# Kernel optimization log

Measured on AMD Instinct MI355X. Metric: run time of the kernel, lower is better.

The kernel has to match this reference:

```python
import jax, jax.numpy as jnp
import numpy as np

NUM_EMBEDDINGS = 1024
EMBEDDING_DIM = 256
COMMITMENT_COST = 0.25


def setup_inputs() -> dict:
    key = jax.random.key(0)
    k1, k2 = jax.random.split(key)
    inputs = jax.random.normal(k1, (64, 1024, EMBEDDING_DIM), dtype=jnp.float32)
    # codebook initialized uniform(-1/K, 1/K) as in the torch module
    embedding = jax.random.uniform(
        k2, (NUM_EMBEDDINGS, EMBEDDING_DIM), dtype=jnp.float32,
        minval=-1.0 / NUM_EMBEDDINGS, maxval=1.0 / NUM_EMBEDDINGS)
    return {"inputs": inputs, "embedding": embedding}


def reference(inputs, embedding):
    # flatten to [N, D]
    D = embedding.shape[1]
    flat = inputs.reshape(-1, D)
    distances = (jnp.sum(flat * flat, axis=1, keepdims=True)
                 + jnp.sum(embedding * embedding, axis=1)
                 - 2.0 * jnp.matmul(flat, embedding.T))
    encoding_indices = jnp.argmin(distances, axis=1)  # [N]
    # one_hot @ embedding == gather; use gather (same math, no NxK one-hot)
    quantized = jnp.take(embedding, encoding_indices, axis=0).reshape(inputs.shape)
    # commitment loss: mse(stop_grad(quantized), inputs)
    e_latent_loss = jnp.mean(jnp.square(jax.lax.stop_gradient(quantized) - inputs))
    loss = COMMITMENT_COST * e_latent_loss
    # straight-through estimator
    quantized = inputs + jax.lax.stop_gradient(quantized - inputs)
    return quantized, loss, encoding_indices.reshape(inputs.shape[:-1])
```

## Files before the change

### kernel.cpp

```cpp
#include <hip/hip_runtime.h>
#include <cfloat>
#include <climits>

#define N_ROWS 65536
#define DIM 256
#define K_CODES 1024
#define N_ELEM 16777216
#define OUT_LOSS_OFF 16777216
#define OUT_IDX_OFF  16777217

#define ROWS_PB 128
#define CT 128
#define EPS_MARGIN 1.5e-4f
#define SHORTLIST_EPS 6e-4f
#define RB 8

#define WS_PARTIALS 0
#define WS_ESQ      8192
#define WS_IDX      12288
#define WS_FLAGCNT  274432
#define WS_FLAGLIST 274436
#define WS_EHI      540672
#define WS_ELO      1064960
#define WS_EHIT     1589248

typedef unsigned short u16;
typedef __attribute__((ext_vector_type(8))) short bf16x8;
typedef __attribute__((ext_vector_type(4))) float f32x4;

__device__ __forceinline__ void glds16(const u16* g, u16* l) {
    __builtin_amdgcn_global_load_lds(
        (const __attribute__((address_space(1))) unsigned int*)(const void*)g,
        (__attribute__((address_space(3))) unsigned int*)(void*)l,
        16, 0, 0);
}

__device__ __forceinline__ void bsplit(float x, u16& h, u16& l) {
    unsigned u = __float_as_uint(x);
    unsigned hb = (u + 0x7fffu + ((u >> 16) & 1u)) >> 16;
    h = (u16)hb;
    float hf = __uint_as_float(hb << 16);
    float lf = x - hf;
    unsigned u2 = __float_as_uint(lf);
    l = (u16)((u2 + 0x7fffu + ((u2 >> 16) & 1u)) >> 16);
}

__device__ __forceinline__ float np_pairwise_sumsq(const float* __restrict__ a) {
    float half[2];
    #pragma unroll
    for (int h = 0; h < 2; ++h) {
        const float* p = a + h * 128;
        float r[8];
        #pragma unroll
        for (int j = 0; j < 8; ++j) r[j] = __fmul_rn(p[j], p[j]);
        for (int i = 8; i < 128; i += 8) {
            #pragma unroll
            for (int j = 0; j < 8; ++j)
                r[j] = __fadd_rn(r[j], __fmul_rn(p[i + j], p[i + j]));
        }
        half[h] = __fadd_rn(__fadd_rn(__fadd_rn(r[0], r[1]), __fadd_rn(r[2], r[3])),
                            __fadd_rn(__fadd_rn(r[4], r[5]), __fadd_rn(r[6], r[7])));
    }
    return __fadd_rn(half[0], half[1]);
}

__global__ void xsplit_kernel(const float* __restrict__ x, u16* __restrict__ xhi,
                              u16* __restrict__ xlo) {
    int i4 = blockIdx.x * 256 + threadIdx.x;
    float4 v = ((const float4*)x)[i4];
    ushort4 h, l;
    bsplit(v.x, h.x, l.x); bsplit(v.y, h.y, l.y);
    bsplit(v.z, h.z, l.z); bsplit(v.w, h.w, l.w);
    ((ushort4*)xhi)[i4] = h;
    ((ushort4*)xlo)[i4] = l;
}

__global__ void esplit_kernel(const float* __restrict__ e, u16* __restrict__ ehi,
                              u16* __restrict__ elo, u16* __restrict__ ehiT) {
    int i4 = blockIdx.x * 256 + threadIdx.x;
    float4 v = ((const float4*)e)[i4];
    ushort4 h, l;
    bsplit(v.x, h.x, l.x); bsplit(v.y, h.y, l.y);
    bsplit(v.z, h.z, l.z); bsplit(v.w, h.w, l.w);
    ((ushort4*)ehi)[i4] = h;
    ((ushort4*)elo)[i4] = l;
    int c = i4 >> 6;
    int f4 = i4 & 63;
    int qid = f4 >> 1;
    ((ushort4*)ehiT)[((size_t)qid * 1024 + c) * 2 + (f4 & 1)] = h;
}

__global__ void esq_kernel(const float* __restrict__ e, float* __restrict__ esq) {
    int c = blockIdx.x * 256 + threadIdx.x;
    if (c < K_CODES) esq[c] = np_pairwise_sumsq(e + c * DIM);
}

__launch_bounds__(256, 2)
__global__ void argmin_kernel(const u16* __restrict__ xhi, const u16* __restrict__ xlo,
                              const u16* __restrict__ ehi, const u16* __restrict__ elo,
                              const float* __restrict__ esq, int* __restrict__ wsIdx,
                              int* __restrict__ flagCnt, int* __restrict__ flagList) {
    __shared__ __align__(16) unsigned char lds[65536];
    __shared__ float esq_s[CT];
    u16* xhiS = (u16*)lds;
    u16* xloS = (u16*)(lds + 16384);
    u16* ehiS = (u16*)(lds + 32768);
    u16* eloS = (u16*)(lds + 49152);

    const int t = threadIdx.x;
    const int w = t >> 6;
    const int l = t & 63;
    const int lane15 = l & 15;
    const int quad = l >> 4;
    const int rowBase = blockIdx.x * ROWS_PB;
    const int waveRowOff = (w >> 1) * 64;
    const int waveColOff = (w & 1) * 64;

    float bv[16], sv[16]; int bi[16];
    #pragma unroll
    for (int i = 0; i < 16; ++i) { bv[i] = FLT_MAX; sv[i] = FLT_MAX; bi[i] = INT_MAX; }

    const u16* src; u16* dst; int gIsX;
    if (w == 0)      { src = xhi; dst = xhiS; gIsX = 1; }
    else if (w == 1) { src = xlo; dst = xloS; gIsX = 1; }
    else if (w == 2) { src = ehi; dst = ehiS; gIsX = 0; }
    else             { src = elo; dst = eloS; gIsX = 0; }
    const int sub = l >> 3;
    const int jb = l & 7;
    const int sb = jb ^ sub;

    for (int ct = 0; ct < 8; ++ct) {
        const int ctBase = ct * CT;
        __syncthreads();
        if (t < CT) esq_s[t] = esq[ctBase + t];

        f32x4 acc[4][4];
        #pragma unroll
        for (int ti = 0; ti < 4; ++ti)
            #pragma unroll
            for (int tj = 0; tj < 4; ++tj) acc[ti][tj] = (f32x4){0.f, 0.f, 0.f, 0.f};

        for (int ch = 0; ch < 4; ++ch) {
            __syncthreads();
            const int gRowBase = gIsX ? rowBase : ctBase;
            #pragma unroll
            for (int i = 0; i < 16; ++i) {
                int r = i * 8 + sub;
                glds16(src + (size_t)(gRowBase + r) * 256 + ch * 64 + sb * 8,
                       dst + i * 512);
            }
            __syncthreads();

            #pragma unroll
            for (int kk = 0; kk < 2; ++kk) {
                bf16x8 ah[4], al4[4], bh[4], bl[4];
                const int blk = kk * 4 + quad;
                #pragma unroll
                for (int ti = 0; ti < 4; ++ti) {
                    int r = waveRowOff + ti * 16 + lane15;
                    int off = r * 64 + ((blk ^ (r & 7)) * 8);
                    ah[ti]  = *(const bf16x8*)(xhiS + off);
                    al4[ti] = *(const bf16x8*)(xloS + off);
                }
                #pragma unroll
                for (int tj = 0; tj < 4; ++tj) {
                    int r = waveColOff + tj * 16 + lane15;
                    int off = r * 64 + ((blk ^ (r & 7)) * 8);
                    bh[tj] = *(const bf16x8*)(ehiS + off);
                    bl[tj] = *(const bf16x8*)(eloS + off);
                }
                #pragma unroll
                for (int ti = 0; ti < 4; ++ti)
                    #pragma unroll
                    for (int tj = 0; tj < 4; ++tj) {
                        acc[ti][tj] = __builtin_amdgcn_mfma_f32_16x16x32_bf16(al4[ti], bh[tj], acc[ti][tj], 0, 0, 0);
                        acc[ti][tj] = __builtin_amdgcn_mfma_f32_16x16x32_bf16(ah[ti], bl[tj], acc[ti][tj], 0, 0, 0);
                        acc[ti][tj] = __builtin_amdgcn_mfma_f32_16x16x32_bf16(ah[ti], bh[tj], acc[ti][tj], 0, 0, 0);
                    }
            }
        }

        #pragma unroll
        for (int tj = 0; tj < 4; ++tj) {
            int cLoc = waveColOff + tj * 16 + lane15;
            float cs = esq_s[cLoc];
            int c = ctBase + cLoc;
            #pragma unroll
            for (int ti = 0; ti < 4; ++ti)
                #pragma unroll
                for (int r4 = 0; r4 < 4; ++r4) {
                    int slot = ti * 4 + r4;
                    float s = fmaf(-2.0f, acc[ti][tj][r4], cs);
                    if (s < bv[slot]) {
                        sv[slot] = bv[slot]; bv[slot] = s; bi[slot] = c;
                    } else if (s < sv[slot]) {
                        sv[slot] = s;
                    }
                }
        }
    }

    __syncthreads();
    float* bvA = (float*)lds;
    float* svA = (float*)(lds + 16384);
    int*   biA = (int*)(lds + 32768);
    const int contrib = (w & 1) * 16 + lane15;
    #pragma unroll
    for (int slot = 0; slot < 16; ++slot) {
        int m = waveRowOff + (slot >> 2) * 16 + quad * 4 + (slot & 3);
        bvA[m * 32 + contrib] = bv[slot];
        svA[m * 32 + contrib] = sv[slot];
        biA[m * 32 + contrib] = bi[slot];
    }
    __syncthreads();

    if (t < ROWS_PB) {
        float bb = FLT_MAX, ss = FLT_MAX;
        int ii = INT_MAX;
        for (int k = 0; k < 32; ++k) {
            float v  = bvA[t * 32 + k];
            int   id = biA[t * 32 + k];
            float s2 = svA[t * 32 + k];
            if (v < bb || (v == bb && id < ii)) {
                ss = fminf(bb, s2);
                bb = v; ii = id;
            } else {
                ss = fminf(ss, v);
            }
        }
        int row = rowBase + t;
        wsIdx[row] = ii;
        if (ss - bb < EPS_MARGIN) {
            int p = atomicAdd(flagCnt, 1);
            flagList[p] = row;
        }
    }
}

__launch_bounds__(256)
__global__ void rescore_kernel(const float* __restrict__ x, const float* __restrict__ e,
                               const u16* __restrict__ ehiT, const float* __restrict__ esq,
                               int* __restrict__ wsIdx, const int* __restrict__ flagCnt,
                               const int* __restrict__ flagList) {
    __shared__ __align__(16) float xsh[RB][DIM];
    __shared__ float Ash[RB];
    __shared__ float minsh[RB][256];
    __shared__ float thrsh[RB];
    __shared__ int scnt[RB];
    __shared__ int slist[RB][32];
    __shared__ float sres[RB][32];
    const int t = threadIdx.x;
    const int cnt = *flagCnt;
    const int ngroups = (cnt + RB - 1) / RB;
    for (int g = blockIdx.x; g < ngroups; g += gridDim.x) {
        const int base = g * RB;
        const int nr = (cnt - base < RB) ? (cnt - base) : RB;
        __syncthreads();
        #pragma unroll
        for (int r = 0; r < RB; ++r)
            xsh[r][t] = (r < nr) ? x[(size_t)flagList[base + r] * DIM + t] : 0.0f;
        if (t < RB) scnt[t] = 0;
        __syncthreads();
        if (t < RB) Ash[t] = np_pairwise_sumsq(xsh[t]);

        float sA[4][RB];
        #pragma unroll
        for (int j = 0; j < 4; ++j)
            #pragma unroll
            for (int r = 0; r < RB; ++r) sA[j][r] = 0.0f;

        const uint4* eT4 = (const uint4*)ehiT;
        for (int q = 0; q < 32; ++q) {
            float4 xq[RB][2];
            #pragma unroll
            for (int r = 0; r < RB; ++r) {
                xq[r][0] = ((const float4*)xsh[r])[2 * q];
                xq[r][1] = ((const float4*)xsh[r])[2 * q + 1];
            }
            #pragma unroll
            for (int j = 0; j < 4; ++j) {
                uint4 uv = eT4[(size_t)q * 1024 + j * 256 + t];
                float e0 = __uint_as_float(uv.x << 16);
                float e1 = __uint_as_float(uv.x & 0xffff0000u);
                float e2 = __uint_as_float(uv.y << 16);
                float e3 = __uint_as_float(uv.y & 0xffff0000u);
                float e4v = __uint_as_float(uv.z << 16);
                float e5 = __uint_as_float(uv.z & 0xffff0000u);
                float e6 = __uint_as_float(uv.w << 16);
                float e7 = __uint_as_float(uv.w & 0xffff0000u);
                #pragma unroll
                for (int r = 0; r < RB; ++r) {
                    float d0 = sA[j][r];
                    d0 = fmaf(e0, xq[r][0].x, d0);
                    d0 = fmaf(e1, xq[r][0].y, d0);
                    d0 = fmaf(e2, xq[r][0].z, d0);
                    d0 = fmaf(e3, xq[r][0].w, d0);
                    d0 = fmaf(e4v, xq[r][1].x, d0);
                    d0 = fmaf(e5, xq[r][1].y, d0);
                    d0 = fmaf(e6, xq[r][1].z, d0);
                    d0 = fmaf(e7, xq[r][1].w, d0);
                    sA[j][r] = d0;
                }
            }
        }
        #pragma unroll
        for (int j = 0; j < 4; ++j) {
            float cs = esq[j * 256 + t];
            #pragma unroll
            for (int r = 0; r < RB; ++r)
                sA[j][r] = fmaf(-2.0f, sA[j][r], cs);
        }
        #pragma unroll
        for (int r = 0; r < RB; ++r)
            minsh[r][t] = fminf(fminf(sA[0][r], sA[1][r]), fminf(sA[2][r], sA[3][r]));
        __syncthreads();
        for (int off = 128; off > 0; off >>= 1) {
            if (t < off) {
                #pragma unroll
                for (int r = 0; r < RB; ++r)
                    minsh[r][t] = fminf(minsh[r][t], minsh[r][t + off]);
            }
            __syncthreads();
        }
        if (t < RB) thrsh[t] = minsh[t][0] + SHORTLIST_EPS;
        __syncthreads();
        #pragma unroll
        for (int j = 0; j < 4; ++j)
            #pragma unroll
            for (int r = 0; r < RB; ++r)
                if (r < nr && sA[j][r] <= thrsh[r]) {
                    int p = atomicAdd(&scnt[r], 1);
                    if (p < 32) slist[r][p] = j * 256 + t;
                }
        __syncthreads();
        {
            int r = t >> 5, k = t & 31;
            int ns = scnt[r] < 32 ? scnt[r] : 32;
            if (r < nr && k < ns) {
                int c = slist[r][k];
                const float4* ec4 = (const float4*)(e + (size_t)c * DIM);
                const float4* xc4 = (const float4*)xsh[r];
                double dot = 0.0;
                #pragma unroll 8
                for (int d4 = 0; d4 < 64; ++d4) {
                    float4 ev = ec4[d4];
                    float4 xv = xc4[d4];
                    dot += (double)ev.x * (double)xv.x + (double)ev.y * (double)xv.y
                         + (double)ev.z * (double)xv.z + (double)ev.w * (double)xv.w;
                }
                float M = (float)dot;
                sres[r][k] = __fsub_rn(__fadd_rn(Ash[r], esq[c]), __fmul_rn(2.0f, M));
            }
        }
        __syncthreads();
        if (t < nr) {
            int ns = scnt[t] < 32 ? scnt[t] : 32;
            float bb = FLT_MAX; int ii = INT_MAX;
            for (int k = 0; k < ns; ++k) {
                float s = sres[t][k]; int c = slist[t][k];
                if (s < bb || (s == bb && c < ii)) { bb = s; ii = c; }
            }
            wsIdx[flagList[base + t]] = ii;
        }
    }
}

__global__ void gather_kernel(const float* __restrict__ x, const float* __restrict__ e,
                              const int* __restrict__ wsIdx, float* __restrict__ out,
                              double* __restrict__ partials) {
    const float4* x4 = (const float4*)x;
    const float4* e4 = (const float4*)e;
    float4* q4 = (float4*)out;
    float* outIdx = out + OUT_IDX_OFF;
    const int tid = blockIdx.x * 256 + threadIdx.x;
    double sse = 0.0;
    #pragma unroll 4
    for (int i = 0; i < 16; ++i) {
        int u = tid + i * 262144;
        int row = u >> 6;
        int c4 = u & 63;
        int idx = wsIdx[row];
        float4 q = e4[idx * 64 + c4];
        float4 xv = x4[u];
        q4[u] = q;
        double dx = (double)q.x - (double)xv.x;
        double dy = (double)q.y - (double)xv.y;
        double dz = (double)q.z - (double)xv.z;
        double dw = (double)q.w - (double)xv.w;
        sse += dx * dx + dy * dy + dz * dz + dw * dw;
    }
    if (tid < N_ROWS) outIdx[tid] = (float)wsIdx[tid];
    #pragma unroll
    for (int m = 1; m < 64; m <<= 1) sse += __shfl_xor(sse, m);
    __shared__ double wsum[4];
    if ((threadIdx.x & 63) == 0) wsum[threadIdx.x >> 6] = sse;
    __syncthreads();
    if (threadIdx.x == 0)
        partials[blockIdx.x] = wsum[0] + wsum[1] + wsum[2] + wsum[3];
}

__global__ void loss_kernel(const double* __restrict__ partials, float* __restrict__ out) {
    __shared__ double sh[256];
    const int t = threadIdx.x;
    double s = partials[t] + partials[t + 256] + partials[t + 512] + partials[t + 768];
    sh[t] = s;
    __syncthreads();
    for (int off = 128; off > 0; off >>= 1) {
        if (t < off) sh[t] += sh[t + off];
        __syncthreads();
    }
    if (t == 0) out[OUT_LOSS_OFF] = (float)(0.25 * sh[0] / (double)N_ELEM);
}

extern "C" void kernel_launch(void* const* d_in, const int* in_sizes, int n_in,
                              void* d_out, int out_size, void* d_ws, size_t ws_size,
                              hipStream_t stream) {
    (void)in_sizes; (void)n_in; (void)out_size; (void)ws_size;
    const float* x = (const float*)d_in[0];
    const float* e = (const float*)d_in[1];
    float* out = (float*)d_out;
    char* ws = (char*)d_ws;
    double* partials = (double*)(ws + WS_PARTIALS);
    float* esq = (float*)(ws + WS_ESQ);
    int* wsIdx = (int*)(ws + WS_IDX);
    int* flagCnt = (int*)(ws + WS_FLAGCNT);
    int* flagList = (int*)(ws + WS_FLAGLIST);
    u16* ehi = (u16*)(ws + WS_EHI);
    u16* elo = (u16*)(ws + WS_ELO);
    u16* ehiT = (u16*)(ws + WS_EHIT);
    u16* xhi = (u16*)d_out;
    u16* xlo = xhi + N_ELEM;

    hipMemsetAsync(flagCnt, 0, sizeof(int), stream);
    xsplit_kernel<<<16384, 256, 0, stream>>>(x, xhi, xlo);
    esplit_kernel<<<256, 256, 0, stream>>>(e, ehi, elo, ehiT);
    esq_kernel<<<4, 256, 0, stream>>>(e, esq);
    argmin_kernel<<<N_ROWS / ROWS_PB, 256, 0, stream>>>(xhi, xlo, ehi, elo, esq,
                                                        wsIdx, flagCnt, flagList);
    rescore_kernel<<<512, 256, 0, stream>>>(x, e, ehiT, esq, wsIdx, flagCnt, flagList);
    gather_kernel<<<1024, 256, 0, stream>>>(x, e, wsIdx, out, partials);
    loss_kernel<<<1, 256, 0, stream>>>(partials, out);
}
```

Baseline: 325.1 us.

## Drop bf16 hi/lo split, use single-bf16 MFMA with wider rescore margin

Replaces the three-MFMA bf16x3 split-precision distance computation with a single bf16 MFMA per tile. The separate x-split pass is removed: the argmin kernel now loads fp32 x directly, converts it to bf16 and stores it in LDS once per block. Codebook fragments are read straight from global/L2 instead of being staged through LDS, which removes the per-chunk barriers. The near-tie margin is widened to absorb the lower precision, which may flag more rows for the exact rescore pass.

```diff
diff --git a/kernel.cpp b/kernel.cpp
--- a/kernel.cpp
+++ b/kernel.cpp
@@ -11,7 +11,7 @@
 
 #define ROWS_PB 128
 #define CT 128
-#define EPS_MARGIN 1.5e-4f
+#define EPS_MARGIN 3.5e-4f
 #define SHORTLIST_EPS 6e-4f
 #define RB 8
 
@@ -21,28 +21,18 @@
 #define WS_FLAGCNT  274432
 #define WS_FLAGLIST 274436
 #define WS_EHI      540672
-#define WS_ELO      1064960
-#define WS_EHIT     1589248
+#define WS_EHIT     1064960
 
 typedef unsigned short u16;
 typedef __attribute__((ext_vector_type(8))) short bf16x8;
 typedef __attribute__((ext_vector_type(4))) float f32x4;
 
-__device__ __forceinline__ void glds16(const u16* g, u16* l) {
-    __builtin_amdgcn_global_load_lds(
-        (const __attribute__((address_space(1))) unsigned int*)(const void*)g,
-        (__attribute__((address_space(3))) unsigned int*)(void*)l,
-        16, 0, 0);
-}
-
-__device__ __forceinline__ void bsplit(float x, u16& h, u16& l) {
-    unsigned u = __float_as_uint(x);
-    unsigned hb = (u + 0x7fffu + ((u >> 16) & 1u)) >> 16;
-    h = (u16)hb;
-    float hf = __uint_as_float(hb << 16);
-    float lf = x - hf;
-    unsigned u2 = __float_as_uint(lf);
-    l = (u16)((u2 + 0x7fffu + ((u2 >> 16) & 1u)) >> 16);
+__device__ __forceinline__ u16 bf16rn(float f) {
+    unsigned u = __float_as_uint(f);
+    return (u16)((u + 0x7fffu + ((u >> 16) & 1u)) >> 16);
+}
+__device__ __forceinline__ unsigned pack2(float a, float b) {
+    return (unsigned)bf16rn(a) | ((unsigned)bf16rn(b) << 16);
 }
 
 __device__ __forceinline__ float np_pairwise_sumsq(const float* __restrict__ a) {
@@ -64,26 +54,13 @@
     return __fadd_rn(half[0], half[1]);
 }
 
-__global__ void xsplit_kernel(const float* __restrict__ x, u16* __restrict__ xhi,
-                              u16* __restrict__ xlo) {
-    int i4 = blockIdx.x * 256 + threadIdx.x;
-    float4 v = ((const float4*)x)[i4];
-    ushort4 h, l;
-    bsplit(v.x, h.x, l.x); bsplit(v.y, h.y, l.y);
-    bsplit(v.z, h.z, l.z); bsplit(v.w, h.w, l.w);
-    ((ushort4*)xhi)[i4] = h;
-    ((ushort4*)xlo)[i4] = l;
-}
-
-__global__ void esplit_kernel(const float* __restrict__ e, u16* __restrict__ ehi,
-                              u16* __restrict__ elo, u16* __restrict__ ehiT) {
+__global__ void eprep_kernel(const float* __restrict__ e, u16* __restrict__ ehi,
+                             u16* __restrict__ ehiT) {
     int i4 = blockIdx.x * 256 + threadIdx.x;
     float4 v = ((const float4*)e)[i4];
-    ushort4 h, l;
-    bsplit(v.x, h.x, l.x); bsplit(v.y, h.y, l.y);
-    bsplit(v.z, h.z, l.z); bsplit(v.w, h.w, l.w);
+    ushort4 h;
+    h.x = bf16rn(v.x); h.y = bf16rn(v.y); h.z = bf16rn(v.z); h.w = bf16rn(v.w);
     ((ushort4*)ehi)[i4] = h;
-    ((ushort4*)elo)[i4] = l;
     int c = i4 >> 6;
     int f4 = i4 & 63;
     int qid = f4 >> 1;
@@ -96,16 +73,11 @@
 }
 
 __launch_bounds__(256, 2)
-__global__ void argmin_kernel(const u16* __restrict__ xhi, const u16* __restrict__ xlo,
-                              const u16* __restrict__ ehi, const u16* __restrict__ elo,
+__global__ void argmin_kernel(const float* __restrict__ x, const u16* __restrict__ ehi,
                               const float* __restrict__ esq, int* __restrict__ wsIdx,
                               int* __restrict__ flagCnt, int* __restrict__ flagList) {
     __shared__ __align__(16) unsigned char lds[65536];
-    __shared__ float esq_s[CT];
-    u16* xhiS = (u16*)lds;
-    u16* xloS = (u16*)(lds + 16384);
-    u16* ehiS = (u16*)(lds + 32768);
-    u16* eloS = (u16*)(lds + 49152);
+    u16* xS = (u16*)lds;
 
     const int t = threadIdx.x;
     const int w = t >> 6;
@@ -116,74 +88,69 @@
     const int waveRowOff = (w >> 1) * 64;
     const int waveColOff = (w & 1) * 64;
 
+    #pragma unroll
+    for (int q = 0; q < 16; ++q) {
+        int id = q * 256 + t;
+        int jb = id & 7;
+        int r = (id >> 3) & 127;
+        int ch = id >> 10;
+        const float4* g = (const float4*)(x + (size_t)(rowBase + r) * 256 + ch * 64 + jb * 8);
+        float4 a = g[0], b = g[1];
+        uint4 p;
+        p.x = pack2(a.x, a.y); p.y = pack2(a.z, a.w);
+        p.z = pack2(b.x, b.y); p.w = pack2(b.z, b.w);
+        *(uint4*)(void*)(xS + ch * 8192 + r * 64 + ((jb ^ (r & 7)) * 8)) = p;
+    }
+    __syncthreads();
+
     float bv[16], sv[16]; int bi[16];
     #pragma unroll
     for (int i = 0; i < 16; ++i) { bv[i] = FLT_MAX; sv[i] = FLT_MAX; bi[i] = INT_MAX; }
 
-    const u16* src; u16* dst; int gIsX;
-    if (w == 0)      { src = xhi; dst = xhiS; gIsX = 1; }
-    else if (w == 1) { src = xlo; dst = xloS; gIsX = 1; }
-    else if (w == 2) { src = ehi; dst = ehiS; gIsX = 0; }
-    else             { src = elo; dst = eloS; gIsX = 0; }
-    const int sub = l >> 3;
-    const int jb = l & 7;
-    const int sb = jb ^ sub;
-
+    const u16* bbase[4];
+    #pragma unroll
+    for (int tj = 0; tj < 4; ++tj)
+        bbase[tj] = ehi + (size_t)(waveColOff + tj * 16 + lane15) * 256 + quad * 8;
+    int rbase[4], rx[4];
+    #pragma unroll
+    for (int ti = 0; ti < 4; ++ti) {
+        int r = waveRowOff + ti * 16 + lane15;
+        rbase[ti] = r * 64; rx[ti] = r & 7;
+    }
+
+    #pragma unroll 1
     for (int ct = 0; ct < 8; ++ct) {
         const int ctBase = ct * CT;
-        __syncthreads();
-        if (t < CT) esq_s[t] = esq[ctBase + t];
-
         f32x4 acc[4][4];
         #pragma unroll
         for (int ti = 0; ti < 4; ++ti)
             #pragma unroll
             for (int tj = 0; tj < 4; ++tj) acc[ti][tj] = (f32x4){0.f, 0.f, 0.f, 0.f};
 
-        for (int ch = 0; ch < 4; ++ch) {
-            __syncthreads();
-            const int gRowBase = gIsX ? rowBase : ctBase;
-            #pragma unroll
-            for (int i = 0; i < 16; ++i) {
-                int r = i * 8 + sub;
-                glds16(src + (size_t)(gRowBase + r) * 256 + ch * 64 + sb * 8,
-                       dst + i * 512);
-            }
-            __syncthreads();
-
-            #pragma unroll
-            for (int kk = 0; kk < 2; ++kk) {
-                bf16x8 ah[4], al4[4], bh[4], bl[4];
-                const int blk = kk * 4 + quad;
+        #pragma unroll
+        for (int ks = 0; ks < 8; ++ks) {
+            bf16x8 af[4], bfv[4];
+            #pragma unroll
+            for (int tj = 0; tj < 4; ++tj)
+                bfv[tj] = *(const bf16x8*)(bbase[tj] + ctBase * 256 + ks * 32);
+            #pragma unroll
+            for (int ti = 0; ti < 4; ++ti) {
+                int off = (ks >> 1) * 8192 + rbase[ti]
+                        + ((((ks & 1) * 4 + quad) ^ rx[ti]) * 8);
+                af[ti] = *(const bf16x8*)(xS + off);
+            }
+            #pragma unroll
+            for (int ti = 0; ti < 4; ++ti)
                 #pragma unroll
-                for (int ti = 0; ti < 4; ++ti) {
-                    int r = waveRowOff + ti * 16 + lane15;
-                    int off = r * 64 + ((blk ^ (r & 7)) * 8);
-                    ah[ti]  = *(const bf16x8*)(xhiS + off);
-                    al4[ti] = *(const bf16x8*)(xloS + off);
-                }
-                #pragma unroll
-                for (int tj = 0; tj < 4; ++tj) {
-                    int r = waveColOff + tj * 16 + lane15;
-                    int off = r * 64 + ((blk ^ (r & 7)) * 8);
-                    bh[tj] = *(const bf16x8*)(ehiS + off);
-                    bl[tj] = *(const bf16x8*)(eloS + off);
-                }
-                #pragma unroll
-                for (int ti = 0; ti < 4; ++ti)
-                    #pragma unroll
-                    for (int tj = 0; tj < 4; ++tj) {
-                        acc[ti][tj] = __builtin_amdgcn_mfma_f32_16x16x32_bf16(al4[ti], bh[tj], acc[ti][tj], 0, 0, 0);
-                        acc[ti][tj] = __builtin_amdgcn_mfma_f32_16x16x32_bf16(ah[ti], bl[tj], acc[ti][tj], 0, 0, 0);
-                        acc[ti][tj] = __builtin_amdgcn_mfma_f32_16x16x32_bf16(ah[ti], bh[tj], acc[ti][tj], 0, 0, 0);
-                    }
-            }
+                for (int tj = 0; tj < 4; ++tj)
+                    acc[ti][tj] = __builtin_amdgcn_mfma_f32_16x16x32_bf16(
+                        af[ti], bfv[tj], acc[ti][tj], 0, 0, 0);
         }
 
         #pragma unroll
         for (int tj = 0; tj < 4; ++tj) {
             int cLoc = waveColOff + tj * 16 + lane15;
-            float cs = esq_s[cLoc];
+            float cs = esq[ctBase + cLoc];
             int c = ctBase + cLoc;
             #pragma unroll
             for (int ti = 0; ti < 4; ++ti)
@@ -426,17 +393,13 @@
     int* flagCnt = (int*)(ws + WS_FLAGCNT);
     int* flagList = (int*)(ws + WS_FLAGLIST);
     u16* ehi = (u16*)(ws + WS_EHI);
-    u16* elo = (u16*)(ws + WS_ELO);
     u16* ehiT = (u16*)(ws + WS_EHIT);
-    u16* xhi = (u16*)d_out;
-    u16* xlo = xhi + N_ELEM;
 
     hipMemsetAsync(flagCnt, 0, sizeof(int), stream);
-    xsplit_kernel<<<16384, 256, 0, stream>>>(x, xhi, xlo);
-    esplit_kernel<<<256, 256, 0, stream>>>(e, ehi, elo, ehiT);
+    eprep_kernel<<<256, 256, 0, stream>>>(e, ehi, ehiT);
     esq_kernel<<<4, 256, 0, stream>>>(e, esq);
-    argmin_kernel<<<N_ROWS / ROWS_PB, 256, 0, stream>>>(xhi, xlo, ehi, elo, esq,
-                                                        wsIdx, flagCnt, flagList);
+    argmin_kernel<<<N_ROWS / ROWS_PB, 256, 0, stream>>>(x, ehi, esq, wsIdx,
+                                                        flagCnt, flagList);
     rescore_kernel<<<512, 256, 0, stream>>>(x, e, ehiT, esq, wsIdx, flagCnt, flagList);
     gather_kernel<<<1024, 256, 0, stream>>>(x, e, wsIdx, out, partials);
     loss_kernel<<<1, 256, 0, stream>>>(partials, out);
```

New measurement: 387.7 us. 19.2% more time.
